# Optimization experiments

Measured on AMD Instinct MI355X. Metric: run time of the kernel, lower is better.

The kernel has to match this reference:

```python
import jax, jax.numpy as jnp
import numpy as np

EPS = 1e-5
DN = ('NCHW', 'OIHW', 'NCHW')


def _conv3x3(x, w):
    return jax.lax.conv_general_dilated(x, w, (1, 1), 'SAME', dimension_numbers=DN)


def _bn_relu(x, g, b):
    # eval-mode BN: running_mean=0, running_var=1
    scale = (g / jnp.sqrt(1.0 + EPS))[None, :, None, None]
    return jax.nn.relu(x * scale + b[None, :, None, None])


def _double_conv(x, w1, g1, b1, w2, g2, b2):
    x = _bn_relu(_conv3x3(x, w1), g1, b1)
    return _bn_relu(_conv3x3(x, w2), g2, b2)


def _up2x_bilinear_align(x):
    # bilinear, align_corners=True, scale_factor=2
    def interp(a, axis, n_in):
        n_out = 2 * n_in
        pos = jnp.arange(n_out, dtype=jnp.float32) * (n_in - 1) / (n_out - 1)
        lo = jnp.floor(pos).astype(jnp.int32)
        hi = jnp.minimum(lo + 1, n_in - 1)
        w = pos - lo.astype(jnp.float32)
        sh = [1, 1, 1, 1]
        sh[axis] = n_out
        w = w.reshape(sh)
        return jnp.take(a, lo, axis=axis) * (1.0 - w) + jnp.take(a, hi, axis=axis) * w
    B, C, H, W = x.shape
    return interp(interp(x, 2, H), 3, W)


def _lstm_dir(seq, Wih, Whh, bih, bhh, reverse):
    # seq: (N, T, C) -> (N, T, Hh); PyTorch gate order i,f,g,o
    Hh = Whh.shape[1]
    xg = jnp.einsum('ntc,gc->ntg', seq, Wih) + (bih + bhh)
    if reverse:
        xg = xg[:, ::-1]
    xg = jnp.swapaxes(xg, 0, 1)  # (T, N, 4H)
    N = seq.shape[0]
    h0 = jnp.zeros((N, Hh), seq.dtype)

    def step(carry, gx):
        h, c = carry
        g = gx + h @ Whh.T
        i, f, gg, o = jnp.split(g, 4, axis=-1)
        c = jax.nn.sigmoid(f) * c + jax.nn.sigmoid(i) * jnp.tanh(gg)
        h = jax.nn.sigmoid(o) * jnp.tanh(c)
        return (h, c), h

    _, hs = jax.lax.scan(step, (h0, h0), xg)
    hs = jnp.swapaxes(hs, 0, 1)  # (N, T, Hh)
    if reverse:
        hs = hs[:, ::-1]
    return hs


def _bilstm(seq, Wf, Uf, bif, bhf, Wb, Ub, bib, bhb):
    return jnp.concatenate([
        _lstm_dir(seq, Wf, Uf, bif, bhf, False),
        _lstm_dir(seq, Wb, Ub, bib, bhb, True),
    ], axis=-1)


def _site_rows(x, lstm):
    # batched version of per-row LSTM: each row is a sequence over W, features C
    B, C, H, W = x.shape
    s = jnp.transpose(x, (0, 2, 3, 1)).reshape(B * H, W, C)
    out = _bilstm(s, *lstm)  # (B*H, W, C) since 2*hidden == C
    return jnp.transpose(out.reshape(B, H, W, C), (0, 3, 1, 2))


def _site_cols(x, lstm):
    # each column is a sequence over H, features C
    B, C, H, W = x.shape
    s = jnp.transpose(x, (0, 3, 2, 1)).reshape(B * W, H, C)
    out = _bilstm(s, *lstm)
    return jnp.transpose(out.reshape(B, W, H, C), (0, 3, 2, 1))


def setup_inputs() -> dict:
    key = jax.random.key(0)
    ks = jax.random.split(key, 24)
    d = {}
    d['x1'] = jax.random.normal(ks[0], (8, 128, 32, 32), jnp.float32)
    d['x2'] = jax.random.normal(ks[1], (8, 128, 64, 64), jnp.float32)
    # bidirectional LSTM: input 256, hidden 128
    d['lstm_Wih_f'] = jax.random.normal(ks[2], (512, 256), jnp.float32) * 0.06
    d['lstm_Whh_f'] = jax.random.normal(ks[3], (512, 128), jnp.float32) * 0.08
    d['lstm_bih_f'] = jax.random.normal(ks[4], (512,), jnp.float32) * 0.05
    d['lstm_bhh_f'] = jax.random.normal(ks[5], (512,), jnp.float32) * 0.05
    d['lstm_Wih_b'] = jax.random.normal(ks[6], (512, 256), jnp.float32) * 0.06
    d['lstm_Whh_b'] = jax.random.normal(ks[7], (512, 128), jnp.float32) * 0.08
    d['lstm_bib_tmp'] = None
    del d['lstm_bib_tmp']
    d['lstm_bih_b'] = jax.random.normal(ks[8], (512,), jnp.float32) * 0.05
    d['lstm_bhh_b'] = jax.random.normal(ks[9], (512,), jnp.float32) * 0.05
    # conv_2 = DoubleConv(512, 256) (mid=256), shared across its two call sites
    d['c2_w1'] = jax.random.normal(ks[10], (256, 512, 3, 3), jnp.float32) * 0.02
    d['c2_g1'] = jax.random.uniform(ks[11], (256,), jnp.float32, 0.5, 1.5)
    d['c2_b1'] = jax.random.normal(ks[12], (256,), jnp.float32) * 0.05
    d['c2_w2'] = jax.random.normal(ks[13], (256, 256, 3, 3), jnp.float32) * 0.03
    d['c2_g2'] = jax.random.uniform(ks[14], (256,), jnp.float32, 0.5, 1.5)
    d['c2_b2'] = jax.random.normal(ks[15], (256,), jnp.float32) * 0.05
    # conv = DoubleConv(256, 128, mid=128)
    d['cv_w1'] = jax.random.normal(ks[16], (128, 256, 3, 3), jnp.float32) * 0.03
    d['cv_g1'] = jax.random.uniform(ks[17], (128,), jnp.float32, 0.5, 1.5)
    d['cv_b1'] = jax.random.normal(ks[18], (128,), jnp.float32) * 0.05
    d['cv_w2'] = jax.random.normal(ks[19], (128, 128, 3, 3), jnp.float32) * 0.04
    d['cv_g2'] = jax.random.uniform(ks[20], (128,), jnp.float32, 0.5, 1.5)
    d['cv_b2'] = jax.random.normal(ks[21], (128,), jnp.float32) * 0.05
    return d


def reference(x1, x2, lstm_Wih_f, lstm_Whh_f, lstm_bih_f, lstm_bhh_f,
              lstm_Wih_b, lstm_Whh_b, lstm_bih_b, lstm_bhh_b,
              c2_w1, c2_g1, c2_b1, c2_w2, c2_g2, c2_b2,
              cv_w1, cv_g1, cv_b1, cv_w2, cv_g2, cv_b2):
    lstm = (lstm_Wih_f, lstm_Whh_f, lstm_bih_f, lstm_bhh_f,
            lstm_Wih_b, lstm_Whh_b, lstm_bih_b, lstm_bhh_b)
    x1u = _up2x_bilinear_align(x1)
    dy = x2.shape[2] - x1u.shape[2]
    dx = x2.shape[3] - x1u.shape[3]
    x1u = jnp.pad(x1u, ((0, 0), (0, 0), (dy // 2, dy - dy // 2), (dx // 2, dx - dx // 2)))
    x = jnp.concatenate([x2, x1u], axis=1)  # (B, 256, 64, 64)
    # site_relation mutates x in-place in torch: rows pass, then cols pass on the
    # row-updated tensor; x_weigth and x_heigth alias the same final tensor.
    x = _site_rows(x, lstm)
    x = _site_cols(x, lstm)
    x_site = jnp.concatenate([x, x], axis=1)  # (B, 512, H, W)
    x_site = _double_conv(x_site, c2_w1, c2_g1, c2_b1, c2_w2, c2_g2, c2_b2)
    x = jnp.concatenate([x, x_site], axis=1)  # (B, 512, H, W)
    x = _double_conv(x, c2_w1, c2_g1, c2_b1, c2_w2, c2_g2, c2_b2)
    x = _double_conv(x, cv_w1, cv_g1, cv_b1, cv_w2, cv_g2, cv_b2)
    return x  # (B, 128, 64, 64)
```

## Files before the change

kernel.cpp:

```cpp
#include <hip/hip_runtime.h>
#include <hip/hip_bf16.h>
#include <math.h>

typedef __bf16 bf16x8 __attribute__((ext_vector_type(8)));
typedef float  f32x4  __attribute__((ext_vector_type(4)));

__device__ __forceinline__ float sigm(float x)  { return 1.f/(1.f+__expf(-x)); }
__device__ __forceinline__ float tanh_f(float x){ return 2.f/(1.f+__expf(-2.f*x)) - 1.f; }
__device__ __forceinline__ float b2f(unsigned short u){
  unsigned int x = ((unsigned int)u) << 16; return __uint_as_float(x);
}
__device__ __forceinline__ unsigned short f2b(float v){
  __hip_bfloat16 h = __float2bfloat16(v); return *(unsigned short*)&h;
}
__device__ __forceinline__ void glds16(const void* g, void* l) {
  __builtin_amdgcn_global_load_lds(
      (const __attribute__((address_space(1))) unsigned int*)g,
      (__attribute__((address_space(3))) unsigned int*)l, 16, 0, 0);
}
__device__ __forceinline__ bf16x8 bzero() {
  bf16x8 v;
  #pragma unroll
  for (int i = 0; i < 8; ++i) v[i] = (__bf16)0.0f;
  return v;
}
__device__ __forceinline__ void barrier_lds() {
  asm volatile("s_waitcnt lgkmcnt(0)\n\ts_barrier" ::: "memory");
}

__global__ __launch_bounds__(256) void k_upcat(const float* __restrict__ x1,
                                               const float* __restrict__ x2,
                                               __hip_bfloat16* __restrict__ X0) {
  int idx = blockIdx.x*256 + threadIdx.x;
  int c = idx & 255;
  int w = (idx >> 8) & 63;
  int h = (idx >> 14) & 63;
  int n = idx >> 20;
  float v;
  if (c < 128) {
    v = x2[((n*128 + c)*64 + h)*64 + w];
  } else {
    int cc = c - 128;
    float py = (h*31.0f)/63.0f;
    int ly = (int)py; int hy = min(ly+1, 31); float fy = py - (float)ly;
    float px = (w*31.0f)/63.0f;
    int lx = (int)px; int hx = min(lx+1, 31); float fx = px - (float)lx;
    const float* p = x1 + (size_t)(n*128 + cc)*1024;
    float v00 = p[ly*32+lx], v01 = p[ly*32+hx];
    float v10 = p[hy*32+lx], v11 = p[hy*32+hx];
    v = (1.f-fy)*((1.f-fx)*v00 + fx*v01) + fy*((1.f-fx)*v10 + fx*v11);
  }
  X0[idx] = __float2bfloat16(v);
}

__global__ __launch_bounds__(256) void k_wih_prep(
    const float* __restrict__ Wf, const float* __restrict__ Wb,
    const float* __restrict__ bif, const float* __restrict__ bhf,
    const float* __restrict__ bib, const float* __restrict__ bhb,
    __hip_bfloat16* __restrict__ wihc, float* __restrict__ biasc) {
  int idx = blockIdx.x*256 + threadIdx.x;
  int n = idx >> 8, k = idx & 255;
  float v = (n < 512) ? Wf[n*256 + k] : Wb[(n-512)*256 + k];
  wihc[idx] = __float2bfloat16(v);
  if (idx < 1024) biasc[idx] = (idx < 512) ? bif[idx] + bhf[idx]
                                           : bib[idx-512] + bhb[idx-512];
}

__global__ __launch_bounds__(256) void k_xg_gemm(
    const __hip_bfloat16* __restrict__ Xin,
    const __hip_bfloat16* __restrict__ Wihc,
    const float* __restrict__ biasc,
    __hip_bfloat16* __restrict__ xg) {
  __shared__ __align__(16) unsigned short sa[128][72];
  __shared__ __align__(16) unsigned short sw[128][72];
  int bx = blockIdx.x;
  int t = bx >> 2, seq0 = (bx & 3) << 7;
  int n0 = blockIdx.y << 7;
  int tid = threadIdx.x, lane = tid & 63, wid = tid >> 6;
  int wm = wid >> 1, wn = wid & 1;
  int l15 = lane & 15, quad = lane >> 4;
  f32x4 acc[4][4];
  #pragma unroll
  for (int i = 0; i < 4; ++i)
    #pragma unroll
    for (int j = 0; j < 4; ++j) acc[i][j] = (f32x4){0.f,0.f,0.f,0.f};

  for (int k0 = 0; k0 < 256; k0 += 64) {
    __syncthreads();
    for (int idx = tid; idx < 2048; idx += 256) {
      int row = idx >> 4, c4 = (idx & 15) << 2;
      *(ushort4*)&sa[row][c4] = *(const ushort4*)((const unsigned short*)Xin +
          (size_t)((seq0 + row)*64 + t)*256 + k0 + c4);
      *(ushort4*)&sw[row][c4] = *(const ushort4*)((const unsigned short*)Wihc +
          (size_t)(n0 + row)*256 + k0 + c4);
    }
    __syncthreads();
    #pragma unroll
    for (int k32 = 0; k32 < 64; k32 += 32) {
      bf16x8 af[4], bfr[4];
      #pragma unroll
      for (int mt = 0; mt < 4; ++mt)
        af[mt] = *(const bf16x8*)&sa[wm*64 + mt*16 + l15][k32 + quad*8];
      #pragma unroll
      for (int nt = 0; nt < 4; ++nt)
        bfr[nt] = *(const bf16x8*)&sw[wn*64 + nt*16 + l15][k32 + quad*8];
      #pragma unroll
      for (int mt = 0; mt < 4; ++mt)
        #pragma unroll
        for (int nt = 0; nt < 4; ++nt)
          acc[mt][nt] = __builtin_amdgcn_mfma_f32_16x16x32_bf16(
              af[mt], bfr[nt], acc[mt][nt], 0, 0, 0);
    }
  }
  #pragma unroll
  for (int nt = 0; nt < 4; ++nt) {
    int cg = n0 + wn*64 + nt*16 + l15;
    int dir = cg >> 9;
    int g   = (cg >> 7) & 3;
    int u   = cg & 127;
    float bias = biasc[cg];
    unsigned short* op = (unsigned short*)xg +
        (size_t)(((dir*64 + t)*4 + g)*512)*128 + u;
    #pragma unroll
    for (int mt = 0; mt < 4; ++mt) {
      int sbase = seq0 + wm*64 + mt*16 + quad*4;
      f32x4 a = acc[mt][nt];
      #pragma unroll
      for (int r = 0; r < 4; ++r)
        op[(size_t)(sbase + r)*128] = f2b(a[r] + bias);
    }
  }
}

__global__ __launch_bounds__(256, 1) void k_lstm_rec(
    const __hip_bfloat16* __restrict__ xg,
    const float* __restrict__ WhhF, const float* __restrict__ WhhB,
    __hip_bfloat16* __restrict__ out) {
  const int dir = blockIdx.y;
  const int sb  = blockIdx.x;
  const float* Whh = dir ? WhhB : WhhF;
  __shared__ __align__(16) unsigned short hs[16][136];
  __shared__ __align__(16) float gv[4][128][4];
  const int tid = threadIdx.x, lane = tid & 63, wv = tid >> 6;
  const int l15 = lane & 15, quad = lane >> 4;

  bf16x8 wf[4][2][4];
  #pragma unroll
  for (int g = 0; g < 4; ++g)
    #pragma unroll
    for (int ut = 0; ut < 2; ++ut) {
      int gate = g*128 + wv*32 + ut*16 + l15;
      #pragma unroll
      for (int kc = 0; kc < 4; ++kc) {
        const float* wp = Whh + (size_t)gate*128 + kc*32 + quad*8;
        float4 w0 = *(const float4*)wp;
        float4 w1 = *(const float4*)(wp + 4);
        bf16x8 f;
        f[0]=(__bf16)w0.x; f[1]=(__bf16)w0.y; f[2]=(__bf16)w0.z; f[3]=(__bf16)w0.w;
        f[4]=(__bf16)w1.x; f[5]=(__bf16)w1.y; f[6]=(__bf16)w1.z; f[7]=(__bf16)w1.w;
        wf[g][ut][kc] = f;
      }
    }
  for (int i = tid; i < 16*136; i += 256) ((unsigned short*)hs)[i] = 0;

  const int u_  = tid & 127;
  const int s0_ = tid >> 7;
  float cst[2] = {0.f, 0.f};

  const unsigned short* xp = (const unsigned short*)xg +
      (size_t)dir*64*4*512*128;
  unsigned short xv[2][4], xn[2][4];
  #define LDX(stp, dst)                                                    \
    {                                                                      \
      int ts_ = (stp) < 64 ? (stp) : 63;                                   \
      int t_  = dir ? 63 - ts_ : ts_;                                      \
      _Pragma("unroll")                                                    \
      for (int j_ = 0; j_ < 2; ++j_) {                                     \
        int s_ = s0_ + j_*2;                                               \
        _Pragma("unroll")                                                  \
        for (int g_ = 0; g_ < 4; ++g_)                                     \
          dst[j_][g_] = xp[(size_t)((t_*4 + g_)*512 + sb*4 + s_)*128 + u_];\
      }                                                                    \
    }
  LDX(0, xv);
  __syncthreads();

  for (int step = 0; step < 64; ++step) {
    int t = dir ? 63 - step : step;
    LDX(step + 1, xn);
    bf16x8 af[2][4];
    #pragma unroll
    for (int mt = 0; mt < 2; ++mt)
      #pragma unroll
      for (int kc = 0; kc < 4; ++kc)
        af[mt][kc] = *(const bf16x8*)&hs[mt*16 + l15][kc*32 + quad*8];
    f32x4 acc[2][4][2];
    #pragma unroll
    for (int mt = 0; mt < 2; ++mt)
      #pragma unroll
      for (int g = 0; g < 4; ++g)
        #pragma unroll
        for (int ut = 0; ut < 2; ++ut) acc[mt][g][ut] = (f32x4){0.f,0.f,0.f,0.f};
    #pragma unroll
    for (int kc = 0; kc < 4; ++kc)
      #pragma unroll
      for (int mt = 0; mt < 2; ++mt)
        #pragma unroll
        for (int g = 0; g < 4; ++g)
          #pragma unroll
          for (int ut = 0; ut < 2; ++ut)
            acc[mt][g][ut] = __builtin_amdgcn_mfma_f32_16x16x32_bf16(
                af[mt][kc], wf[g][ut][kc], acc[mt][g][ut], 0, 0, 0);
    if (quad == 0) {
      #pragma unroll
      for (int ut = 0; ut < 2; ++ut) {
        int u = wv*32 + ut*16 + l15;
        #pragma unroll
        for (int r = 0; r < 4; ++r) {
          float4 q;
          q.x = acc[0][0][ut][r]; q.y = acc[0][1][ut][r];
          q.z = acc[0][2][ut][r]; q.w = acc[0][3][ut][r];
          *(float4*)&gv[r][u][0] = q;
        }
      }
    }
    barrier_lds();
    #pragma unroll
    for (int j = 0; j < 2; ++j) {
      int s = s0_ + j*2;
      float4 gq = *(const float4*)&gv[s][u_][0];
      float I = gq.x + b2f(xv[j][0]);
      float F = gq.y + b2f(xv[j][1]);
      float G = gq.z + b2f(xv[j][2]);
      float O = gq.w + b2f(xv[j][3]);
      float cv = sigm(F)*cst[j] + sigm(I)*tanh_f(G);
      float hv = sigm(O)*tanh_f(cv);
      cst[j] = cv;
      unsigned short hb = f2b(hv);
      hs[s][u_] = hb;
      int gs = sb*4 + s;
      ((unsigned short*)out)[(size_t)(((gs >> 6)*64 + t)*64 + (gs & 63))*256
                             + dir*128 + u_] = hb;
    }
    barrier_lds();
    #pragma unroll
    for (int j = 0; j < 2; ++j)
      #pragma unroll
      for (int g = 0; g < 4; ++g) xv[j][g] = xn[j][g];
  }
  #undef LDX
}

__global__ __launch_bounds__(256) void k_wrefmt_bf16(const float* __restrict__ src,
                                                     __hip_bfloat16* __restrict__ dst,
                                                     int Ci, int Co, int fold) {
  int idx = blockIdx.x*256 + threadIdx.x;
  int total = 9*Ci*Co;
  if (idx >= total) return;
  int ci = idx % Ci;
  int co = (idx / Ci) % Co;
  int k  = idx / (Ci*Co);
  int CiS = fold ? Ci*2 : Ci;
  float v = src[(size_t)(co*CiS + ci)*9 + k];
  if (fold) v += src[(size_t)(co*CiS + ci + Ci)*9 + k];
  dst[idx] = __float2bfloat16(v);
}

__global__ __launch_bounds__(256, 2) void k_conv3_v3(
    const __hip_bfloat16* __restrict__ inA, const __hip_bfloat16* __restrict__ inB,
    const __hip_bfloat16* __restrict__ wgt,
    const float* __restrict__ gam, const float* __restrict__ bet,
    float* __restrict__ outF, __hip_bfloat16* __restrict__ outB,
    int Cin, int Co, int nchw) {
  __shared__ __align__(16) unsigned short si[6][64][64];
  __shared__ __align__(16) unsigned short sw[3][64][64];
  int bx = blockIdx.x;
  int n  = bx >> 4;
  int h0 = (bx & 15) << 2;
  int co0 = blockIdx.y << 6;
  int tid = threadIdx.x;
  int lane = tid & 63;
  int wvid = tid >> 6;
  int l15 = lane & 15, quad = lane >> 4;
  int pl = lane >> 3, pc = lane & 7;

  f32x4 acc[4][4];
  #pragma unroll
  for (int i = 0; i < 4; ++i)
    #pragma unroll
    for (int j = 0; j < 4; ++j) acc[i][j] = (f32x4){0.f,0.f,0.f,0.f};

  int cs = inB ? 256 : Cin;
  for (int ci0 = 0; ci0 < Cin; ci0 += 64) {
    const unsigned short* src = (const unsigned short*)inA; int cb = ci0;
    if (inB && ci0 >= 256) { src = (const unsigned short*)inB; cb = ci0 - 256; }
    __syncthreads();
    #pragma unroll
    for (int j = 0; j < 12; ++j) {
      int s = wvid + j*4;
      int row = s >> 3, grp = s & 7;
      int ih = h0 + row - 1;
      if (ih >= 0 && ih <= 63) {
        const unsigned short* gsrc = src + (size_t)((n*64 + ih)*64)*cs + cb;
        int iw = grp*8 + pl;
        int lc = pc ^ (iw & 7);
        glds16(gsrc + (size_t)iw*cs + lc*8, &si[row][grp*8][0]);
      } else {
        uint4 z = {0,0,0,0};
        *(uint4*)((unsigned short*)&si[row][grp*8][0] + lane*8) = z;
      }
    }
    for (int ky = 0; ky < 3; ++ky) {
      if (ky) __syncthreads();
      {
        const unsigned short* wk = (const unsigned short*)wgt +
            (size_t)(ky*3*Co + co0)*Cin + ci0;
        #pragma unroll
        for (int j = 0; j < 6; ++j) {
          int s = wvid + j*4;
          int kx = s >> 3, cg = s & 7;
          int co = cg*8 + pl;
          int lc = pc ^ (co & 7);
          glds16(wk + (size_t)(kx*Co + co)*Cin + lc*8, &sw[kx][cg*8][0]);
        }
      }
      __syncthreads();
      int row = wvid + ky;
      #pragma unroll
      for (int kx = 0; kx < 3; ++kx) {
        #pragma unroll
        for (int k32 = 0; k32 < 2; ++k32) {
          bf16x8 af[4], bfr[4];
          #pragma unroll
          for (int mt = 0; mt < 4; ++mt) {
            int iw = mt*16 + l15 + kx - 1;
            int iwc = iw & 63;
            int pcc = (k32*4 + quad) ^ (iwc & 7);
            af[mt] = *(const bf16x8*)&si[row][iwc][pcc*8];
            if ((kx == 0 && mt == 0 && l15 == 0) ||
                (kx == 2 && mt == 3 && l15 == 15))
              af[mt] = bzero();
          }
          #pragma unroll
          for (int nt = 0; nt < 4; ++nt) {
            int co = nt*16 + l15;
            int pcc = (k32*4 + quad) ^ (co & 7);
            bfr[nt] = *(const bf16x8*)&sw[kx][co][pcc*8];
          }
          #pragma unroll
          for (int mt = 0; mt < 4; ++mt)
            #pragma unroll
            for (int nt = 0; nt < 4; ++nt)
              acc[mt][nt] = __builtin_amdgcn_mfma_f32_16x16x32_bf16(
                  af[mt], bfr[nt], acc[mt][nt], 0, 0, 0);
        }
      }
    }
  }
  const float kS = 0.9999950000374997f;
  int h = h0 + wvid;
  #pragma unroll
  for (int nt = 0; nt < 4; ++nt) {
    int co = co0 + nt*16 + l15;
    float scale = gam[co]*kS, bb = bet[co];
    #pragma unroll
    for (int mt = 0; mt < 4; ++mt) {
      f32x4 a = acc[mt][nt];
      #pragma unroll
      for (int r = 0; r < 4; ++r) {
        int w = mt*16 + quad*4 + r;
        float v = fmaf(a[r], scale, bb);
        v = v > 0.f ? v : 0.f;
        if (nchw) outF[(size_t)((n*Co + co)*64 + h)*64 + w] = v;
        else      outB[(size_t)((n*64 + h)*64 + w)*Co + co] = __float2bfloat16(v);
      }
    }
  }
}

extern "C" void kernel_launch(void* const* d_in, const int* in_sizes, int n_in,
                              void* d_out, int out_size, void* d_ws, size_t ws_size,
                              hipStream_t stream) {
  const float* x1    = (const float*)d_in[0];
  const float* x2    = (const float*)d_in[1];
  const float* Wih_f = (const float*)d_in[2];
  const float* Whh_f = (const float*)d_in[3];
  const float* bih_f = (const float*)d_in[4];
  const float* bhh_f = (const float*)d_in[5];
  const float* Wih_b = (const float*)d_in[6];
  const float* Whh_b = (const float*)d_in[7];
  const float* bih_b = (const float*)d_in[8];
  const float* bhh_b = (const float*)d_in[9];
  const float* c2_w1 = (const float*)d_in[10];
  const float* c2_g1 = (const float*)d_in[11];
  const float* c2_b1 = (const float*)d_in[12];
  const float* c2_w2 = (const float*)d_in[13];
  const float* c2_g2 = (const float*)d_in[14];
  const float* c2_b2 = (const float*)d_in[15];
  const float* cv_w1 = (const float*)d_in[16];
  const float* cv_g1 = (const float*)d_in[17];
  const float* cv_b1 = (const float*)d_in[18];
  const float* cv_w2 = (const float*)d_in[19];
  const float* cv_g2 = (const float*)d_in[20];
  const float* cv_b2 = (const float*)d_in[21];

  char* base = (char*)d_ws;
  const size_t SLOTB = 16777216ull;
  __hip_bfloat16* Xb  = (__hip_bfloat16*)(base);
  __hip_bfloat16* Sb  = (__hip_bfloat16*)(base);
  __hip_bfloat16* XG  = (__hip_bfloat16*)(base + SLOTB);
  __hip_bfloat16* D2  = (__hip_bfloat16*)(base + SLOTB);
  __hip_bfloat16* D2b = (__hip_bfloat16*)(base + 2*SLOTB);
  __hip_bfloat16* RT  = (__hip_bfloat16*)(base + SLOTB + 67108864ull);
  __hip_bfloat16* D1  = RT;
  char* wq = base + SLOTB + 67108864ull + SLOTB;
  __hip_bfloat16* wihc  = (__hip_bfloat16*)wq;
  float*          biasc = (float*)(wq + 524288);
  char* cw = wq + 528384;
  __hip_bfloat16* w1f    = (__hip_bfloat16*)(cw);
  __hip_bfloat16* w1full = (__hip_bfloat16*)(cw + 1179648);
  __hip_bfloat16* w2r    = (__hip_bfloat16*)(cw + 3538944);
  __hip_bfloat16* wv1    = (__hip_bfloat16*)(cw + 4718592);
  __hip_bfloat16* wv2    = (__hip_bfloat16*)(cw + 5308416);

  k_wih_prep<<<1024, 256, 0, stream>>>(Wih_f, Wih_b, bih_f, bhh_f, bih_b, bhh_b,
                                       wihc, biasc);
  k_wrefmt_bf16<<<(9*256*256+255)/256, 256, 0, stream>>>(c2_w1, w1f,    256, 256, 1);
  k_wrefmt_bf16<<<(9*512*256+255)/256, 256, 0, stream>>>(c2_w1, w1full, 512, 256, 0);
  k_wrefmt_bf16<<<(9*256*256+255)/256, 256, 0, stream>>>(c2_w2, w2r,    256, 256, 0);
  k_wrefmt_bf16<<<(9*256*128+255)/256, 256, 0, stream>>>(cv_w1, wv1,    256, 128, 0);
  k_wrefmt_bf16<<<(9*128*128+255)/256, 256, 0, stream>>>(cv_w2, wv2,    128, 128, 0);

  k_upcat<<<32768, 256, 0, stream>>>(x1, x2, Xb);

  k_xg_gemm<<<dim3(256, 8), 256, 0, stream>>>(Xb, wihc, biasc, XG);
  k_lstm_rec<<<dim3(128, 2), 256, 0, stream>>>(XG, Whh_f, Whh_b, RT);
  k_xg_gemm<<<dim3(256, 8), 256, 0, stream>>>(RT, wihc, biasc, XG);
  k_lstm_rec<<<dim3(128, 2), 256, 0, stream>>>(XG, Whh_f, Whh_b, Sb);

  k_conv3_v3<<<dim3(128,4), 256, 0, stream>>>(Sb, nullptr, w1f, c2_g1, c2_b1,
                                              nullptr, D1, 256, 256, 0);
  k_conv3_v3<<<dim3(128,4), 256, 0, stream>>>(D1, nullptr, w2r, c2_g2, c2_b2,
                                              nullptr, D2, 256, 256, 0);
  k_conv3_v3<<<dim3(128,4), 256, 0, stream>>>(Sb, D2, w1full, c2_g1, c2_b1,
                                              nullptr, D2b, 512, 256, 0);
  k_conv3_v3<<<dim3(128,4), 256, 0, stream>>>(D2b, nullptr, w2r, c2_g2, c2_b2,
                                              nullptr, D1, 256, 256, 0);
  k_conv3_v3<<<dim3(128,2), 256, 0, stream>>>(D1, nullptr, wv1, cv_g1, cv_b1,
                                              nullptr, D2, 256, 128, 0);
  k_conv3_v3<<<dim3(128,2), 256, 0, stream>>>(D2, nullptr, wv2, cv_g2, cv_b2,
                                              (float*)d_out, nullptr, 128, 128, 1);
}
```

Measured before the change: 659.6 us.

## Add 512-thread conv kernel with 128-wide output-channel tiles for 256-channel convs

Adds a new implicit-GEMM 3x3 conv kernel in which each 512-thread block computes 4 rows × 64 columns × 128 output channels. It stages a 6-row input halo and per-ky weight slices in LDS using swizzled global-to-LDS loads, and switches the four 256-output-channel convs to it with half as many blocks in the channel dimension. The wider channel tile lets each staged input tile be reused across twice as many output channels, cutting input reloads. In exchange the kernel uses large LDS and one block per CU, which reduces the number of blocks and the latency hiding available.

```diff
diff --git a/kernel.cpp b/kernel.cpp
--- a/kernel.cpp
+++ b/kernel.cpp
@@ -373,6 +373,118 @@
         v = v > 0.f ? v : 0.f;
         if (nchw) outF[(size_t)((n*Co + co)*64 + h)*64 + w] = v;
         else      outB[(size_t)((n*64 + h)*64 + w)*Co + co] = __float2bfloat16(v);
+      }
+    }
+  }
+}
+
+__global__ __launch_bounds__(512, 1) void k_conv3_v5(
+    const __hip_bfloat16* __restrict__ inA, const __hip_bfloat16* __restrict__ inB,
+    const __hip_bfloat16* __restrict__ wgt,
+    const float* __restrict__ gam, const float* __restrict__ bet,
+    __hip_bfloat16* __restrict__ outB, int Cin, int Co) {
+  __shared__ __align__(16) unsigned short si[6][64][64];
+  __shared__ __align__(16) unsigned short sw[3][128][64];
+  int bx = blockIdx.x;
+  int n  = bx >> 4;
+  int h0 = (bx & 15) << 2;
+  int co0 = blockIdx.y << 7;
+  int tid = threadIdx.x;
+  int lane = tid & 63;
+  int wid  = tid >> 6;
+  int wm = wid >> 1;
+  int wn = wid & 1;
+  int l15 = lane & 15, quad = lane >> 4;
+  int pl = lane >> 3, pc = lane & 7;
+
+  f32x4 acc[4][4];
+  #pragma unroll
+  for (int i = 0; i < 4; ++i)
+    #pragma unroll
+    for (int j = 0; j < 4; ++j) acc[i][j] = (f32x4){0.f,0.f,0.f,0.f};
+
+  int cs = inB ? 256 : Cin;
+  for (int ci0 = 0; ci0 < Cin; ci0 += 64) {
+    const unsigned short* src = (const unsigned short*)inA; int cb = ci0;
+    if (inB && ci0 >= 256) { src = (const unsigned short*)inB; cb = ci0 - 256; }
+    __syncthreads();
+    #pragma unroll
+    for (int j = 0; j < 6; ++j) {
+      int s = wid + j*8;
+      int row = s >> 3, grp = s & 7;
+      int ih = h0 + row - 1;
+      if (ih >= 0 && ih <= 63) {
+        const unsigned short* gsrc = src + (size_t)((n*64 + ih)*64)*cs + cb;
+        int iw = grp*8 + pl;
+        int lc = pc ^ (iw & 7);
+        glds16(gsrc + (size_t)iw*cs + lc*8, &si[row][grp*8][0]);
+      } else {
+        uint4 z = {0,0,0,0};
+        *(uint4*)((unsigned short*)&si[row][grp*8][0] + lane*8) = z;
+      }
+    }
+    for (int ky = 0; ky < 3; ++ky) {
+      if (ky) __syncthreads();
+      {
+        const unsigned short* wk = (const unsigned short*)wgt +
+            (size_t)(ky*3*Co + co0)*Cin + ci0;
+        #pragma unroll
+        for (int j = 0; j < 6; ++j) {
+          int s = wid + j*8;
+          int kx = s >> 4, cg = s & 15;
+          int co = cg*8 + pl;
+          int lc = pc ^ (co & 7);
+          glds16(wk + (size_t)(kx*Co + co)*Cin + lc*8, &sw[kx][cg*8][0]);
+        }
+      }
+      __syncthreads();
+      int row = wm + ky;
+      #pragma unroll
+      for (int kx = 0; kx < 3; ++kx) {
+        #pragma unroll
+        for (int k32 = 0; k32 < 2; ++k32) {
+          bf16x8 af[4], bfr[4];
+          #pragma unroll
+          for (int mt = 0; mt < 4; ++mt) {
+            int iw = mt*16 + l15 + kx - 1;
+            int iwc = iw & 63;
+            int pcc = (k32*4 + quad) ^ (iwc & 7);
+            af[mt] = *(const bf16x8*)&si[row][iwc][pcc*8];
+            if ((kx == 0 && mt == 0 && l15 == 0) ||
+                (kx == 2 && mt == 3 && l15 == 15))
+              af[mt] = bzero();
+          }
+          #pragma unroll
+          for (int nt = 0; nt < 4; ++nt) {
+            int co = wn*64 + nt*16 + l15;
+            int pcc = (k32*4 + quad) ^ (co & 7);
+            bfr[nt] = *(const bf16x8*)&sw[kx][co][pcc*8];
+          }
+          #pragma unroll
+          for (int mt = 0; mt < 4; ++mt)
+            #pragma unroll
+            for (int nt = 0; nt < 4; ++nt)
+              acc[mt][nt] = __builtin_amdgcn_mfma_f32_16x16x32_bf16(
+                  af[mt], bfr[nt], acc[mt][nt], 0, 0, 0);
+        }
+      }
+    }
+  }
+  const float kS = 0.9999950000374997f;
+  int h = h0 + wm;
+  #pragma unroll
+  for (int nt = 0; nt < 4; ++nt) {
+    int co = co0 + wn*64 + nt*16 + l15;
+    float scale = gam[co]*kS, bb = bet[co];
+    #pragma unroll
+    for (int mt = 0; mt < 4; ++mt) {
+      f32x4 a = acc[mt][nt];
+      #pragma unroll
+      for (int r = 0; r < 4; ++r) {
+        int w = mt*16 + quad*4 + r;
+        float v = fmaf(a[r], scale, bb);
+        v = v > 0.f ? v : 0.f;
+        outB[(size_t)((n*64 + h)*64 + w)*Co + co] = __float2bfloat16(v);
       }
     }
   }
@@ -438,14 +550,14 @@
   k_xg_gemm<<<dim3(256, 8), 256, 0, stream>>>(RT, wihc, biasc, XG);
   k_lstm_rec<<<dim3(128, 2), 256, 0, stream>>>(XG, Whh_f, Whh_b, Sb);
 
-  k_conv3_v3<<<dim3(128,4), 256, 0, stream>>>(Sb, nullptr, w1f, c2_g1, c2_b1,
-                                              nullptr, D1, 256, 256, 0);
-  k_conv3_v3<<<dim3(128,4), 256, 0, stream>>>(D1, nullptr, w2r, c2_g2, c2_b2,
-                                              nullptr, D2, 256, 256, 0);
-  k_conv3_v3<<<dim3(128,4), 256, 0, stream>>>(Sb, D2, w1full, c2_g1, c2_b1,
-                                              nullptr, D2b, 512, 256, 0);
-  k_conv3_v3<<<dim3(128,4), 256, 0, stream>>>(D2b, nullptr, w2r, c2_g2, c2_b2,
-                                              nullptr, D1, 256, 256, 0);
+  k_conv3_v5<<<dim3(128,2), 512, 0, stream>>>(Sb, nullptr, w1f, c2_g1, c2_b1,
+                                              D1, 256, 256);
+  k_conv3_v5<<<dim3(128,2), 512, 0, stream>>>(D1, nullptr, w2r, c2_g2, c2_b2,
+                                              D2, 256, 256);
+  k_conv3_v5<<<dim3(128,2), 512, 0, stream>>>(Sb, D2, w1full, c2_g1, c2_b1,
+                                              D2b, 512, 256);
+  k_conv3_v5<<<dim3(128,2), 512, 0, stream>>>(D2b, nullptr, w2r, c2_g2, c2_b2,
+                                              D1, 256, 256);
   k_conv3_v3<<<dim3(128,2), 256, 0, stream>>>(D1, nullptr, wv1, cv_g1, cv_b1,
                                               nullptr, D2, 256, 128, 0);
   k_conv3_v3<<<dim3(128,2), 256, 0, stream>>>(D2, nullptr, wv2, cv_g2, cv_b2,
```

New measurement: 663.9 us. Within noise of the previous version (+0.6%).
